# Kernel tuning notes

Hardware: AMD Instinct MI355X
Metric: run time of the kernel (lower is better)

The kernel has to match this reference:

```python
import jax, jax.numpy as jnp
import numpy as np

NUM_NODES = 50000
NUM_EDGES = 800000
NUM_LABEL_EDGES = 100000
F_IN, F_HID, F_OUT = 128, 128, 64


def gcn_conv(x, src, dst, W, b, n):
    # PyG GCNConv: h = x @ W; add self-loops; symmetric normalization
    # deg counted on destination (col), including self-loop (+1).
    h = x @ W
    deg = jax.ops.segment_sum(jnp.ones(src.shape, h.dtype), dst, num_segments=n) + 1.0
    dinv = jax.lax.rsqrt(deg)  # deg >= 1 always (self-loop)
    norm = dinv[src] * dinv[dst]                       # [E]
    agg = jax.ops.segment_sum(h[src] * norm[:, None], dst, num_segments=n)
    agg = agg + h * (dinv * dinv)[:, None]             # self-loop term dinv[i]^2 * h[i]
    return agg + b


def setup_inputs() -> dict:
    key = jax.random.key(0)
    ks = jax.random.split(key, 9)
    x = jax.random.normal(ks[0], (NUM_NODES, F_IN), dtype=jnp.float32)
    edge_index = jax.random.randint(ks[1], (2, NUM_EDGES), 0, NUM_NODES, dtype=jnp.int64)
    edge_label_index = jax.random.randint(ks[2], (2, NUM_LABEL_EDGES), 0, NUM_NODES, dtype=jnp.int64)
    def glorot(k, fi, fo):
        s = (6.0 / (fi + fo)) ** 0.5
        return jax.random.uniform(k, (fi, fo), jnp.float32, -s, s)
    return {
        "x": x,
        "edge_index": edge_index,
        "edge_label_index": edge_label_index,
        "W1": glorot(ks[3], F_IN, F_HID),  "b1": jnp.zeros((F_HID,), jnp.float32),
        "W2": glorot(ks[4], F_HID, F_HID), "b2": jnp.zeros((F_HID,), jnp.float32),
        "W3": glorot(ks[5], F_HID, F_OUT), "b3": jnp.zeros((F_OUT,), jnp.float32),
    }


def reference(x, edge_index, edge_label_index, W1, b1, W2, b2, W3, b3):
    src, dst = edge_index[0], edge_index[1]
    z = jax.nn.relu(gcn_conv(x, src, dst, W1, b1, NUM_NODES))
    z = jax.nn.relu(gcn_conv(z, src, dst, W2, b2, NUM_NODES))
    z = gcn_conv(z, src, dst, W3, b3, NUM_NODES)
    # decode: dot product of endpoint embeddings per label edge
    return jnp.sum(z[edge_label_index[0]] * z[edge_label_index[1]], axis=-1)
```

## Files before the change

### kernel.cpp

```cpp
#include <hip/hip_runtime.h>
#include <hip/hip_bf16.h>
#include <stdint.h>

#define NN 50000
#define NE 800000
#define NL 100000
#define F_IN 128
#define F_HID 128
#define F_OUT 64
#define SLOTS 64

#define NB 196
#define BSH 8
#define BCAP 5376

typedef __attribute__((ext_vector_type(8))) short bf16x8;
typedef __attribute__((ext_vector_type(4))) float f32x4;

__device__ __forceinline__ float bf2f(unsigned short u) {
    union { unsigned int i; float f; } c; c.i = ((unsigned int)u) << 16; return c.f;
}
__device__ __forceinline__ unsigned short f2bf(float f) {
    union { float f; unsigned int i; } c; c.f = f;
    unsigned int u = c.i + (0x7fffu + ((c.i >> 16) & 1u));
    return (unsigned short)(u >> 16);
}
__device__ __forceinline__ bf16x8 pack8(float4 lo, float4 hi) {
    bf16x8 r;
    r[0] = (short)f2bf(lo.x); r[1] = (short)f2bf(lo.y);
    r[2] = (short)f2bf(lo.z); r[3] = (short)f2bf(lo.w);
    r[4] = (short)f2bf(hi.x); r[5] = (short)f2bf(hi.y);
    r[6] = (short)f2bf(hi.z); r[7] = (short)f2bf(hi.w);
    return r;
}


__global__ void wprep(const float* __restrict__ W1, const float* __restrict__ W2,
                      const float* __restrict__ W3, unsigned short* __restrict__ Wt,
                      int* __restrict__ cursor) {
    if (blockIdx.x == 0 && threadIdx.x < NB) cursor[threadIdx.x] = 0;
    int idx = blockIdx.x * 256 + threadIdx.x;
    const float* W; unsigned short* O; int base, Mloc;
    if (idx < 16384)      { W = W1; O = Wt;         base = idx;         Mloc = 128; }
    else if (idx < 32768) { W = W2; O = Wt + 16384; base = idx - 16384; Mloc = 128; }
    else                  { W = W3; O = Wt + 32768; base = idx - 32768; Mloc = 64;  }
    int n = base >> 7, k = base & 127;
    O[base] = f2bf(W[k * Mloc + n]);
}


__global__ __launch_bounds__(256) void bin_edges(
        const int* __restrict__ src, const int* __restrict__ dst,
        int* __restrict__ cursor, unsigned int* __restrict__ binbuf) {
    __shared__ int hcnt[NB];
    __shared__ int hbase[NB];
    int tid = threadIdx.x;
    if (tid < NB) hcnt[tid] = 0;
    __syncthreads();
    int e0 = blockIdx.x * 2048;
#pragma unroll
    for (int r = 0; r < 8; ++r) {
        int e = e0 + r * 256 + tid;
        if (e < NE) atomicAdd(&hcnt[dst[e] >> BSH], 1);
    }
    __syncthreads();
    if (tid < NB) { hbase[tid] = atomicAdd(&cursor[tid], hcnt[tid]); hcnt[tid] = 0; }
    __syncthreads();
#pragma unroll
    for (int r = 0; r < 8; ++r) {
        int e = e0 + r * 256 + tid;
        if (e < NE) {
            int d = dst[e], s = src[e];
            int b = d >> BSH;
            int p = hbase[b] + atomicAdd(&hcnt[b], 1);
            if (p < BCAP)
                binbuf[(size_t)b * BCAP + p] = (unsigned int)s | ((unsigned int)d << 16);
        }
    }
}


__global__ __launch_bounds__(256) void build_csr(
        const unsigned int* __restrict__ binbuf, const int* __restrict__ cursor,
        int* __restrict__ deg, unsigned short* __restrict__ colp) {
    __shared__ unsigned short lcol[256 * SLOTS];
    __shared__ int ldeg[256];
    int tid = threadIdx.x;
    int blk = blockIdx.x;
    int base = blk << BSH;
    int nNodes = min(256, NN - base);
    ldeg[tid] = 0;
    __syncthreads();
    int cnt = min(cursor[blk], BCAP);
    for (int e = tid; e < cnt; e += 256) {
        unsigned int pk = binbuf[(size_t)blk * BCAP + e];
        int d = (int)(pk >> 16) - base;
        int p = atomicAdd(&ldeg[d], 1);
        if (p < SLOTS) lcol[d * SLOTS + p] = (unsigned short)(pk & 0xffffu);
    }
    __syncthreads();
    if (tid < nNodes) deg[base + tid] = ldeg[tid];
    uint4* gout = (uint4*)(colp + (size_t)base * SLOTS);
    const uint4* lin = (const uint4*)lcol;
    for (int i = tid; i < nNodes * 8; i += 256) gout[i] = lin[i];
}


template <int M_, int AFP32>
__global__ __launch_bounds__(256) void gemm_mfma(
        const void* __restrict__ Av, const unsigned short* __restrict__ Wt,
        const int* __restrict__ deg, unsigned short* __restrict__ Outb, int N) {
    constexpr int K = 128;
    constexpr int NT = M_ / 16;
    int lane = threadIdx.x & 63;
    int wave = threadIdx.x >> 6;
    int m    = lane & 15;
    int quad = lane >> 4;
    int rowA = blockIdx.x * 64 + wave * 16 + m;
    int rA   = min(rowA, N - 1);

    bf16x8 afr[4];
    if (AFP32) {
        const float* A = (const float*)Av;
        const float* p = A + (size_t)rA * K + quad * 8;
#pragma unroll
        for (int s = 0; s < 4; ++s) {
            float4 lo = *(const float4*)(p + s * 32);
            float4 hi = *(const float4*)(p + s * 32 + 4);
            afr[s] = pack8(lo, hi);
        }
    } else {
        const unsigned short* A = (const unsigned short*)Av;
#pragma unroll
        for (int s = 0; s < 4; ++s)
            afr[s] = *(const bf16x8*)(A + (size_t)rA * K + s * 32 + quad * 8);
    }

    f32x4 acc[NT];
#pragma unroll
    for (int t = 0; t < NT; ++t) { acc[t][0] = 0.f; acc[t][1] = 0.f; acc[t][2] = 0.f; acc[t][3] = 0.f; }

#pragma unroll
    for (int t = 0; t < NT; ++t) {
        const unsigned short* wp = Wt + (size_t)(t * 16 + m) * K + quad * 8;
#pragma unroll
        for (int s = 0; s < 4; ++s) {
            bf16x8 bfr = *(const bf16x8*)(wp + s * 32);
            acc[t] = __builtin_amdgcn_mfma_f32_16x16x32_bf16(afr[s], bfr, acc[t], 0, 0, 0);
        }
    }

    int outRowBase = blockIdx.x * 64 + wave * 16 + quad * 4;
    float di[4];
#pragma unroll
    for (int i = 0; i < 4; ++i) {
        int rr = min(outRowBase + i, N - 1);
        di[i] = rsqrtf((float)deg[rr] + 1.0f);
    }
#pragma unroll
    for (int t = 0; t < NT; ++t) {
#pragma unroll
        for (int i = 0; i < 4; ++i) {
            int rr = outRowBase + i;
            if (rr < N)
                Outb[(size_t)rr * M_ + t * 16 + m] = f2bf(acc[t][i] * di[i]);
        }
    }
}


template <int F, int RELU>
__global__ __launch_bounds__(256) void aggregate(
        const unsigned short* __restrict__ hs, const int* __restrict__ deg,
        const unsigned short* __restrict__ colp, const float* __restrict__ bias,
        unsigned short* __restrict__ out, int n) {
    int wave = threadIdx.x >> 6;
    int lane = threadIdx.x & 63;
    int node = blockIdx.x * 4 + wave;
    if (node >= n) return;

    float acc0 = 0.f, acc1 = 0.f;
    if (F == 128) {
        unsigned int v = *(const unsigned int*)(hs + (size_t)node * F + lane * 2);
        acc0 = bf2f((unsigned short)v); acc1 = bf2f((unsigned short)(v >> 16));
    } else {
        acc0 = bf2f(hs[(size_t)node * F + lane]);
    }

    int cnt = min(deg[node], SLOTS);
    int myIdx = (lane < cnt) ? (int)colp[(size_t)node * SLOTS + lane] : 0;
    int j = 0;
    for (; j + 8 <= cnt; j += 8) {
        int i0 = __shfl(myIdx, j + 0, 64);
        int i1 = __shfl(myIdx, j + 1, 64);
        int i2 = __shfl(myIdx, j + 2, 64);
        int i3 = __shfl(myIdx, j + 3, 64);
        int i4 = __shfl(myIdx, j + 4, 64);
        int i5 = __shfl(myIdx, j + 5, 64);
        int i6 = __shfl(myIdx, j + 6, 64);
        int i7 = __shfl(myIdx, j + 7, 64);
        if (F == 128) {
            unsigned int v0 = *(const unsigned int*)(hs + (size_t)i0 * F + lane * 2);
            unsigned int v1 = *(const unsigned int*)(hs + (size_t)i1 * F + lane * 2);
            unsigned int v2 = *(const unsigned int*)(hs + (size_t)i2 * F + lane * 2);
            unsigned int v3 = *(const unsigned int*)(hs + (size_t)i3 * F + lane * 2);
            unsigned int v4 = *(const unsigned int*)(hs + (size_t)i4 * F + lane * 2);
            unsigned int v5 = *(const unsigned int*)(hs + (size_t)i5 * F + lane * 2);
            unsigned int v6 = *(const unsigned int*)(hs + (size_t)i6 * F + lane * 2);
            unsigned int v7 = *(const unsigned int*)(hs + (size_t)i7 * F + lane * 2);
            acc0 += ((bf2f((unsigned short)v0) + bf2f((unsigned short)v1)) +
                     (bf2f((unsigned short)v2) + bf2f((unsigned short)v3))) +
                    ((bf2f((unsigned short)v4) + bf2f((unsigned short)v5)) +
                     (bf2f((unsigned short)v6) + bf2f((unsigned short)v7)));
            acc1 += ((bf2f((unsigned short)(v0 >> 16)) + bf2f((unsigned short)(v1 >> 16))) +
                     (bf2f((unsigned short)(v2 >> 16)) + bf2f((unsigned short)(v3 >> 16)))) +
                    ((bf2f((unsigned short)(v4 >> 16)) + bf2f((unsigned short)(v5 >> 16))) +
                     (bf2f((unsigned short)(v6 >> 16)) + bf2f((unsigned short)(v7 >> 16))));
        } else {
            float v0 = bf2f(hs[(size_t)i0 * F + lane]);
            float v1 = bf2f(hs[(size_t)i1 * F + lane]);
            float v2 = bf2f(hs[(size_t)i2 * F + lane]);
            float v3 = bf2f(hs[(size_t)i3 * F + lane]);
            float v4 = bf2f(hs[(size_t)i4 * F + lane]);
            float v5 = bf2f(hs[(size_t)i5 * F + lane]);
            float v6 = bf2f(hs[(size_t)i6 * F + lane]);
            float v7 = bf2f(hs[(size_t)i7 * F + lane]);
            acc0 += ((v0 + v1) + (v2 + v3)) + ((v4 + v5) + (v6 + v7));
        }
    }
    for (; j < cnt; ++j) {
        int idx = __shfl(myIdx, j, 64);
        if (F == 128) {
            unsigned int v = *(const unsigned int*)(hs + (size_t)idx * F + lane * 2);
            acc0 += bf2f((unsigned short)v);
            acc1 += bf2f((unsigned short)(v >> 16));
        } else {
            acc0 += bf2f(hs[(size_t)idx * F + lane]);
        }
    }

    float di = rsqrtf((float)deg[node] + 1.0f);
    if (F == 128) {
        float o0 = di * acc0 + bias[lane * 2];
        float o1 = di * acc1 + bias[lane * 2 + 1];
        if (RELU) { o0 = fmaxf(o0, 0.f); o1 = fmaxf(o1, 0.f); }
        unsigned int w = (unsigned int)f2bf(o0) | ((unsigned int)f2bf(o1) << 16);
        *(unsigned int*)(out + (size_t)node * F + lane * 2) = w;
    } else {
        float o = di * acc0 + bias[lane];
        if (RELU) o = fmaxf(o, 0.f);
        out[(size_t)node * F + lane] = f2bf(o);
    }
}


__global__ __launch_bounds__(256) void decode(
        const unsigned short* __restrict__ z, const int* __restrict__ ls,
        const int* __restrict__ ld, float* __restrict__ out, int nl) {
    int wave = threadIdx.x >> 6;
    int lane = threadIdx.x & 63;
    int e = blockIdx.x * 4 + wave;
    if (e >= nl) return;
    float p = bf2f(z[(size_t)ls[e] * F_OUT + lane]) * bf2f(z[(size_t)ld[e] * F_OUT + lane]);
#pragma unroll
    for (int off = 32; off > 0; off >>= 1) p += __shfl_down(p, off, 64);
    if (lane == 0) out[e] = p;
}


static inline size_t align256(size_t x) { return (x + 255) & ~(size_t)255; }

extern "C" void kernel_launch(void* const* d_in, const int* in_sizes, int n_in,
                              void* d_out, int out_size, void* d_ws, size_t ws_size,
                              hipStream_t stream) {
    const float* x  = (const float*)d_in[0];
    const int*   ei = (const int*)d_in[1];
    const int*   li = (const int*)d_in[2];
    const float* W1 = (const float*)d_in[3];
    const float* b1 = (const float*)d_in[4];
    const float* W2 = (const float*)d_in[5];
    const float* b2 = (const float*)d_in[6];
    const float* W3 = (const float*)d_in[7];
    const float* b3 = (const float*)d_in[8];
    float* out = (float*)d_out;

    const int* src = ei;
    const int* dst = ei + NE;
    const int* ls = li;
    const int* ld = li + NL;

    char* ws = (char*)d_ws;
    size_t off = 0;
    int* deg    = (int*)(ws + off); off += align256(NN * 4);
    int* cursor = (int*)(ws + off); off += align256(NB * 4);
    unsigned int* binbuf = (unsigned int*)(ws + off); off += align256((size_t)NB * BCAP * 4);
    unsigned short* colp = (unsigned short*)(ws + off); off += align256((size_t)NN * SLOTS * 2);
    unsigned short* Wtb  = (unsigned short*)(ws + off); off += align256(40960 * 2);
    unsigned short* bufH = (unsigned short*)(ws + off); off += align256((size_t)NN * F_HID * 2);
    unsigned short* bufP = (unsigned short*)(ws + off); off += align256((size_t)NN * F_HID * 2);

    const int aggBlocks = (NN + 3) / 4;
    const int gemmBlocks = (NN + 63) / 64;
    const int binBlocks = (NE + 2047) / 2048;

    wprep<<<160, 256, 0, stream>>>(W1, W2, W3, Wtb, cursor);
    bin_edges<<<binBlocks, 256, 0, stream>>>(src, dst, cursor, binbuf);
    build_csr<<<NB, 256, 0, stream>>>(binbuf, cursor, deg, colp);

    gemm_mfma<128, 1><<<gemmBlocks, 256, 0, stream>>>(x, Wtb, deg, bufH, NN);
    aggregate<128, 1><<<aggBlocks, 256, 0, stream>>>(bufH, deg, colp, b1, bufP, NN);

    gemm_mfma<128, 0><<<gemmBlocks, 256, 0, stream>>>(bufP, Wtb + 16384, deg, bufH, NN);
    aggregate<128, 1><<<aggBlocks, 256, 0, stream>>>(bufH, deg, colp, b2, bufP, NN);

    gemm_mfma<64, 0><<<gemmBlocks, 256, 0, stream>>>(bufP, Wtb + 32768, deg, bufH, NN);
    aggregate<64, 0><<<aggBlocks, 256, 0, stream>>>(bufH, deg, colp, b3, bufP, NN);

    decode<<<(NL + 3) / 4, 256, 0, stream>>>(bufP, ls, ld, out, NL);
}
```

Baseline: 275.0 us.

## Split aggregation wave into two half-waves gathering wider rows; add nontemporal loads/stores

The aggregate kernel now has each half-wave (32 lanes) gather a whole neighbor row with 8-byte (or 4-byte for F=64) loads. The two halves process alternating neighbors and are combined with a cross-half shuffle. Masking replaces the scalar tail loop. Nontemporal load/store builtins are also applied to binning, CSR build, GEMM inputs/outputs, aggregation outputs and decode output to reduce cache pollution. The risks are masked wasted loads for odd counts, and nontemporal hints hurting reuse for data that is read again soon, such as the GEMM output gathered by aggregate.

```diff
diff --git a/kernel.cpp b/kernel.cpp
--- a/kernel.cpp
+++ b/kernel.cpp
@@ -16,22 +16,19 @@
 
 typedef __attribute__((ext_vector_type(8))) short bf16x8;
 typedef __attribute__((ext_vector_type(4))) float f32x4;
-
-__device__ __forceinline__ float bf2f(unsigned short u) {
-    union { unsigned int i; float f; } c; c.i = ((unsigned int)u) << 16; return c.f;
-}
+typedef __attribute__((ext_vector_type(2))) unsigned int u32x2;
+typedef __attribute__((ext_vector_type(4))) unsigned int u32x4;
+typedef __attribute__((ext_vector_type(4))) float f32x4v;
+
+__device__ __forceinline__ float asf(unsigned int u) {
+    union { unsigned int i; float f; } c; c.i = u; return c.f;
+}
+__device__ __forceinline__ float bflo(unsigned int x) { return asf(x << 16); }
+__device__ __forceinline__ float bfhi(unsigned int x) { return asf(x & 0xffff0000u); }
 __device__ __forceinline__ unsigned short f2bf(float f) {
     union { float f; unsigned int i; } c; c.f = f;
     unsigned int u = c.i + (0x7fffu + ((c.i >> 16) & 1u));
     return (unsigned short)(u >> 16);
-}
-__device__ __forceinline__ bf16x8 pack8(float4 lo, float4 hi) {
-    bf16x8 r;
-    r[0] = (short)f2bf(lo.x); r[1] = (short)f2bf(lo.y);
-    r[2] = (short)f2bf(lo.z); r[3] = (short)f2bf(lo.w);
-    r[4] = (short)f2bf(hi.x); r[5] = (short)f2bf(hi.y);
-    r[6] = (short)f2bf(hi.z); r[7] = (short)f2bf(hi.w);
-    return r;
 }
 
 
@@ -74,7 +71,9 @@
             int b = d >> BSH;
             int p = hbase[b] + atomicAdd(&hcnt[b], 1);
             if (p < BCAP)
-                binbuf[(size_t)b * BCAP + p] = (unsigned int)s | ((unsigned int)d << 16);
+                __builtin_nontemporal_store(
+                    (unsigned int)s | ((unsigned int)d << 16),
+                    &binbuf[(size_t)b * BCAP + p]);
         }
     }
 }
@@ -93,15 +92,15 @@
     __syncthreads();
     int cnt = min(cursor[blk], BCAP);
     for (int e = tid; e < cnt; e += 256) {
-        unsigned int pk = binbuf[(size_t)blk * BCAP + e];
+        unsigned int pk = __builtin_nontemporal_load(&binbuf[(size_t)blk * BCAP + e]);
         int d = (int)(pk >> 16) - base;
         int p = atomicAdd(&ldeg[d], 1);
         if (p < SLOTS) lcol[d * SLOTS + p] = (unsigned short)(pk & 0xffffu);
     }
     __syncthreads();
     if (tid < nNodes) deg[base + tid] = ldeg[tid];
-    uint4* gout = (uint4*)(colp + (size_t)base * SLOTS);
-    const uint4* lin = (const uint4*)lcol;
+    u32x4* gout = (u32x4*)(colp + (size_t)base * SLOTS);
+    const u32x4* lin = (const u32x4*)lcol;
     for (int i = tid; i < nNodes * 8; i += 256) gout[i] = lin[i];
 }
 
@@ -125,15 +124,21 @@
         const float* p = A + (size_t)rA * K + quad * 8;
 #pragma unroll
         for (int s = 0; s < 4; ++s) {
-            float4 lo = *(const float4*)(p + s * 32);
-            float4 hi = *(const float4*)(p + s * 32 + 4);
-            afr[s] = pack8(lo, hi);
+            f32x4v lo = __builtin_nontemporal_load((const f32x4v*)(p + s * 32));
+            f32x4v hi = __builtin_nontemporal_load((const f32x4v*)(p + s * 32 + 4));
+            bf16x8 r;
+            r[0] = (short)f2bf(lo[0]); r[1] = (short)f2bf(lo[1]);
+            r[2] = (short)f2bf(lo[2]); r[3] = (short)f2bf(lo[3]);
+            r[4] = (short)f2bf(hi[0]); r[5] = (short)f2bf(hi[1]);
+            r[6] = (short)f2bf(hi[2]); r[7] = (short)f2bf(hi[3]);
+            afr[s] = r;
         }
     } else {
         const unsigned short* A = (const unsigned short*)Av;
 #pragma unroll
         for (int s = 0; s < 4; ++s)
-            afr[s] = *(const bf16x8*)(A + (size_t)rA * K + s * 32 + quad * 8);
+            afr[s] = __builtin_nontemporal_load(
+                (const bf16x8*)(A + (size_t)rA * K + s * 32 + quad * 8));
     }
 
     f32x4 acc[NT];
@@ -163,7 +168,9 @@
         for (int i = 0; i < 4; ++i) {
             int rr = outRowBase + i;
             if (rr < N)
-                Outb[(size_t)rr * M_ + t * 16 + m] = f2bf(acc[t][i] * di[i]);
+                __builtin_nontemporal_store(
+                    f2bf(acc[t][i] * di[i]),
+                    &Outb[(size_t)rr * M_ + t * 16 + m]);
         }
     }
 }
@@ -178,78 +185,83 @@
     int lane = threadIdx.x & 63;
     int node = blockIdx.x * 4 + wave;
     if (node >= n) return;
-
-    float acc0 = 0.f, acc1 = 0.f;
-    if (F == 128) {
-        unsigned int v = *(const unsigned int*)(hs + (size_t)node * F + lane * 2);
-        acc0 = bf2f((unsigned short)v); acc1 = bf2f((unsigned short)(v >> 16));
-    } else {
-        acc0 = bf2f(hs[(size_t)node * F + lane]);
+    int sub  = lane & 31;
+    int half = lane >> 5;
+    constexpr int PF = (F == 128) ? 4 : 2;
+
+    float acc[PF] = {};
+    if (half == 0) {
+        if (F == 128) {
+            u32x2 v = *(const u32x2*)(hs + (size_t)node * F + sub * 4);
+            acc[0] = bflo(v[0]); acc[1] = bfhi(v[0]);
+            acc[2] = bflo(v[1]); acc[3] = bfhi(v[1]);
+        } else {
+            unsigned int v = *(const unsigned int*)(hs + (size_t)node * F + sub * 2);
+            acc[0] = bflo(v); acc[1] = bfhi(v);
+        }
     }
 
     int cnt = min(deg[node], SLOTS);
     int myIdx = (lane < cnt) ? (int)colp[(size_t)node * SLOTS + lane] : 0;
-    int j = 0;
-    for (; j + 8 <= cnt; j += 8) {
-        int i0 = __shfl(myIdx, j + 0, 64);
-        int i1 = __shfl(myIdx, j + 1, 64);
-        int i2 = __shfl(myIdx, j + 2, 64);
-        int i3 = __shfl(myIdx, j + 3, 64);
-        int i4 = __shfl(myIdx, j + 4, 64);
-        int i5 = __shfl(myIdx, j + 5, 64);
-        int i6 = __shfl(myIdx, j + 6, 64);
-        int i7 = __shfl(myIdx, j + 7, 64);
+    int P = (cnt + 1) >> 1;
+    for (int p = 0; p < P; p += 8) {
+        int ev[8], iv[8];
+#pragma unroll
+        for (int u = 0; u < 8; ++u) {
+            ev[u] = 2 * (p + u) + half;
+            iv[u] = __shfl(myIdx, ev[u], 64);
+        }
         if (F == 128) {
-            unsigned int v0 = *(const unsigned int*)(hs + (size_t)i0 * F + lane * 2);
-            unsigned int v1 = *(const unsigned int*)(hs + (size_t)i1 * F + lane * 2);
-            unsigned int v2 = *(const unsigned int*)(hs + (size_t)i2 * F + lane * 2);
-            unsigned int v3 = *(const unsigned int*)(hs + (size_t)i3 * F + lane * 2);
-            unsigned int v4 = *(const unsigned int*)(hs + (size_t)i4 * F + lane * 2);
-            unsigned int v5 = *(const unsigned int*)(hs + (size_t)i5 * F + lane * 2);
-            unsigned int v6 = *(const unsigned int*)(hs + (size_t)i6 * F + lane * 2);
-            unsigned int v7 = *(const unsigned int*)(hs + (size_t)i7 * F + lane * 2);
-            acc0 += ((bf2f((unsigned short)v0) + bf2f((unsigned short)v1)) +
-                     (bf2f((unsigned short)v2) + bf2f((unsigned short)v3))) +
-                    ((bf2f((unsigned short)v4) + bf2f((unsigned short)v5)) +
-                     (bf2f((unsigned short)v6) + bf2f((unsigned short)v7)));
-            acc1 += ((bf2f((unsigned short)(v0 >> 16)) + bf2f((unsigned short)(v1 >> 16))) +
-                     (bf2f((unsigned short)(v2 >> 16)) + bf2f((unsigned short)(v3 >> 16)))) +
-                    ((bf2f((unsigned short)(v4 >> 16)) + bf2f((unsigned short)(v5 >> 16))) +
-                     (bf2f((unsigned short)(v6 >> 16)) + bf2f((unsigned short)(v7 >> 16))));
+            u32x2 vv[8];
+#pragma unroll
+            for (int u = 0; u < 8; ++u)
+                vv[u] = *(const u32x2*)(hs + (size_t)iv[u] * F + sub * 4);
+#pragma unroll
+            for (int u = 0; u < 8; ++u) {
+                unsigned int mx = (ev[u] < cnt) ? 0xffffffffu : 0u;
+                unsigned int x = vv[u][0] & mx, y = vv[u][1] & mx;
+                acc[0] += bflo(x); acc[1] += bfhi(x);
+                acc[2] += bflo(y); acc[3] += bfhi(y);
+            }
         } else {
-            float v0 = bf2f(hs[(size_t)i0 * F + lane]);
-            float v1 = bf2f(hs[(size_t)i1 * F + lane]);
-            float v2 = bf2f(hs[(size_t)i2 * F + lane]);
-            float v3 = bf2f(hs[(size_t)i3 * F + lane]);
-            float v4 = bf2f(hs[(size_t)i4 * F + lane]);
-            float v5 = bf2f(hs[(size_t)i5 * F + lane]);
-            float v6 = bf2f(hs[(size_t)i6 * F + lane]);
-            float v7 = bf2f(hs[(size_t)i7 * F + lane]);
-            acc0 += ((v0 + v1) + (v2 + v3)) + ((v4 + v5) + (v6 + v7));
-        }
-    }
-    for (; j < cnt; ++j) {
-        int idx = __shfl(myIdx, j, 64);
+            unsigned int vv[8];
+#pragma unroll
+            for (int u = 0; u < 8; ++u)
+                vv[u] = *(const unsigned int*)(hs + (size_t)iv[u] * F + sub * 2);
+#pragma unroll
+            for (int u = 0; u < 8; ++u) {
+                unsigned int mx = (ev[u] < cnt) ? 0xffffffffu : 0u;
+                unsigned int x = vv[u] & mx;
+                acc[0] += bflo(x); acc[1] += bfhi(x);
+            }
+        }
+    }
+
+#pragma unroll
+    for (int k = 0; k < PF; ++k) acc[k] += __shfl_xor(acc[k], 32, 64);
+
+    if (half == 0) {
+        float di = rsqrtf((float)deg[node] + 1.0f);
         if (F == 128) {
-            unsigned int v = *(const unsigned int*)(hs + (size_t)idx * F + lane * 2);
-            acc0 += bf2f((unsigned short)v);
-            acc1 += bf2f((unsigned short)(v >> 16));
+            float o0 = di * acc[0] + bias[sub * 4 + 0];
+            float o1 = di * acc[1] + bias[sub * 4 + 1];
+            float o2 = di * acc[2] + bias[sub * 4 + 2];
+            float o3 = di * acc[3] + bias[sub * 4 + 3];
+            if (RELU) {
+                o0 = fmaxf(o0, 0.f); o1 = fmaxf(o1, 0.f);
+                o2 = fmaxf(o2, 0.f); o3 = fmaxf(o3, 0.f);
+            }
+            u32x2 w;
+            w[0] = (unsigned int)f2bf(o0) | ((unsigned int)f2bf(o1) << 16);
+            w[1] = (unsigned int)f2bf(o2) | ((unsigned int)f2bf(o3) << 16);
+            __builtin_nontemporal_store(w, (u32x2*)(out + (size_t)node * F + sub * 4));
         } else {
-            acc0 += bf2f(hs[(size_t)idx * F + lane]);
-        }
-    }
-
-    float di = rsqrtf((float)deg[node] + 1.0f);
-    if (F == 128) {
-        float o0 = di * acc0 + bias[lane * 2];
-        float o1 = di * acc1 + bias[lane * 2 + 1];
-        if (RELU) { o0 = fmaxf(o0, 0.f); o1 = fmaxf(o1, 0.f); }
-        unsigned int w = (unsigned int)f2bf(o0) | ((unsigned int)f2bf(o1) << 16);
-        *(unsigned int*)(out + (size_t)node * F + lane * 2) = w;
-    } else {
-        float o = di * acc0 + bias[lane];
-        if (RELU) o = fmaxf(o, 0.f);
-        out[(size_t)node * F + lane] = f2bf(o);
+            float o0 = di * acc[0] + bias[sub * 2 + 0];
+            float o1 = di * acc[1] + bias[sub * 2 + 1];
+            if (RELU) { o0 = fmaxf(o0, 0.f); o1 = fmaxf(o1, 0.f); }
+            unsigned int w = (unsigned int)f2bf(o0) | ((unsigned int)f2bf(o1) << 16);
+            __builtin_nontemporal_store(w, (unsigned int*)(out + (size_t)node * F + sub * 2));
+        }
     }
 }
 
@@ -261,10 +273,11 @@
     int lane = threadIdx.x & 63;
     int e = blockIdx.x * 4 + wave;
     if (e >= nl) return;
-    float p = bf2f(z[(size_t)ls[e] * F_OUT + lane]) * bf2f(z[(size_t)ld[e] * F_OUT + lane]);
+    float p = bflo((unsigned int)z[(size_t)ls[e] * F_OUT + lane]) *
+              bflo((unsigned int)z[(size_t)ld[e] * F_OUT + lane]);
 #pragma unroll
     for (int off = 32; off > 0; off >>= 1) p += __shfl_down(p, off, 64);
-    if (lane == 0) out[e] = p;
+    if (lane == 0) __builtin_nontemporal_store(p, &out[e]);
 }
 
 
```

Result: slower. 281.5 us (+2.4%).
